# Kernel optimization log

Hardware: AMD Instinct MI355X
Metric: run time of the kernel (lower is better)

Reference implementation:

```python
import jax, jax.numpy as jnp
import numpy as np

G = 4      # num_groups
I = 128    # per-group input dim  (input_dim // num_groups)
H = 128    # per-group hidden dim (hidden_dim // num_groups)
B, T = 32, 1000


def setup_inputs() -> dict:
    key = jax.random.key(0)
    k0, k1, k2, k3, k4 = jax.random.split(key, 5)
    s = 1.0 / np.sqrt(H)  # PyTorch GRU init scale
    x = jax.random.normal(k0, (B, T, G * I), dtype=jnp.float32)
    w_ih = jax.random.uniform(k1, (G, 3 * H, I), jnp.float32, -s, s)
    w_hh = jax.random.uniform(k2, (G, 3 * H, H), jnp.float32, -s, s)
    b_ih = jax.random.uniform(k3, (G, 3 * H), jnp.float32, -s, s)
    b_hh = jax.random.uniform(k4, (G, 3 * H), jnp.float32, -s, s)
    return {"x": x, "w_ih": w_ih, "w_hh": w_hh, "b_ih": b_ih, "b_hh": b_hh}


def reference(x, w_ih, w_hh, b_ih, b_hh):
    # x: [B, T, G*I]. Chunking along dim 2 == reshape to [B, T, G, I].
    Bx, Tx, _ = x.shape
    xg = x.reshape(Bx, Tx, G, I)
    # Precompute input projections for all timesteps/groups (block-diagonal GEMM).
    gi = jnp.einsum('btgi,gki->btgk', xg, w_ih) + b_ih  # [B, T, G, 3H]

    def step(h, gi_t):
        # h: [B, G, H]; gi_t: [B, G, 3H]
        gh = jnp.einsum('bgh,gkh->bgk', h, w_hh) + b_hh  # [B, G, 3H]
        i_r, i_z, i_n = jnp.split(gi_t, 3, axis=-1)
        h_r, h_z, h_n = jnp.split(gh, 3, axis=-1)
        r = jax.nn.sigmoid(i_r + h_r)
        z = jax.nn.sigmoid(i_z + h_z)
        n = jnp.tanh(i_n + r * h_n)
        h_new = (1.0 - z) * n + z * h
        return h_new, h_new

    h0 = jnp.zeros((Bx, G, H), dtype=x.dtype)
    _, ys = jax.lax.scan(step, h0, jnp.swapaxes(gi, 0, 1))  # [T, B, G, H]
    # Concat of group outputs along dim 2 == reshape [B, T, G*H].
    return jnp.swapaxes(ys, 0, 1).reshape(Bx, Tx, G * H)
```

## Files before the change

### kernel.cpp

```cpp
#include <hip/hip_runtime.h>
#include <hip/hip_bf16.h>

#define NG 4
#define ID 128
#define HD 128
#define TH 384
#define NB 32
#define NT 1000
#define XW (NG*ID)
#define OW (NG*HD)

typedef _Float16 v8h __attribute__((ext_vector_type(8)));
typedef __attribute__((ext_vector_type(4))) float v4f;

__device__ __forceinline__ float sigm(float v) {
    return __fdividef(1.f, 1.f + __expf(-v));
}
__device__ __forceinline__ float tanh_(float v) {
    v = fminf(fmaxf(v, -15.f), 15.f);
    float e2 = __expf(2.f * v);
    return __fdividef(e2 - 1.f, e2 + 1.f);
}
__device__ __forceinline__ float sel4(v4f a, int s) {
    float x01 = (s & 1) ? a[1] : a[0];
    float x23 = (s & 1) ? a[3] : a[2];
    return (s & 2) ? x23 : x01;
}

__global__ __launch_bounds__(256) void gi_gemm4(
    const float* __restrict__ x,
    const float* __restrict__ w_ih,
    const float* __restrict__ b_ih,
    _Float16* __restrict__ gi_ws)
{
    const int tid = threadIdx.x;
    const int w   = tid >> 6, l = tid & 63;
    const int lr  = l & 15, lq = l >> 4;
    const int g   = blockIdx.z;
    const int b   = blockIdx.y >> 3;
    const int tt  = blockIdx.y & 7;
    const int gate = blockIdx.x;
    const int n0  = gate * 128 + (w >> 1) * 64;
    const int t0  = tt * 128 + (w & 1) * 64;

    v4f acc[4][4];
    #pragma unroll
    for (int mi = 0; mi < 4; ++mi)
        #pragma unroll
        for (int ni = 0; ni < 4; ++ni)
            acc[mi][ni] = (v4f){0.f, 0.f, 0.f, 0.f};

    #pragma unroll
    for (int kf = 0; kf < 4; ++kf) {
        v8h bf[4], af[4];
        #pragma unroll
        for (int ni = 0; ni < 4; ++ni) {
            const float* p = &w_ih[(size_t)(g * TH + n0 + ni * 16 + lr) * ID + kf * 32 + lq * 8];
            float4 f0 = *reinterpret_cast<const float4*>(p);
            float4 f1 = *reinterpret_cast<const float4*>(p + 4);
            v8h v;
            v[0]=(_Float16)f0.x; v[1]=(_Float16)f0.y; v[2]=(_Float16)f0.z; v[3]=(_Float16)f0.w;
            v[4]=(_Float16)f1.x; v[5]=(_Float16)f1.y; v[6]=(_Float16)f1.z; v[7]=(_Float16)f1.w;
            bf[ni] = v;
        }
        #pragma unroll
        for (int mi = 0; mi < 4; ++mi) {
            int trow = t0 + mi * 16 + lr;
            int tl = trow < NT ? trow : NT - 1;
            const float* p = &x[((size_t)b * NT + tl) * XW + g * ID + kf * 32 + lq * 8];
            float4 f0 = *reinterpret_cast<const float4*>(p);
            float4 f1 = *reinterpret_cast<const float4*>(p + 4);
            v8h v;
            v[0]=(_Float16)f0.x; v[1]=(_Float16)f0.y; v[2]=(_Float16)f0.z; v[3]=(_Float16)f0.w;
            v[4]=(_Float16)f1.x; v[5]=(_Float16)f1.y; v[6]=(_Float16)f1.z; v[7]=(_Float16)f1.w;
            af[mi] = v;
        }
        #pragma unroll
        for (int mi = 0; mi < 4; ++mi)
            #pragma unroll
            for (int ni = 0; ni < 4; ++ni)
                acc[mi][ni] = __builtin_amdgcn_mfma_f32_16x16x32_f16(
                    af[mi], bf[ni], acc[mi][ni], 0, 0, 0);
    }

    const size_t rbase = (size_t)(b * NG + g) * NT;
    #pragma unroll
    for (int ni = 0; ni < 4; ++ni) {
        const int col = n0 + ni * 16 + lr;
        const float bias = b_ih[g * TH + col];
        const int jj = col & 127;
        const int off = (gate == 0) ? jj * 2 : (gate == 1) ? jj * 2 + 1 : 256 + jj;
        #pragma unroll
        for (int mi = 0; mi < 4; ++mi) {
            #pragma unroll
            for (int r = 0; r < 4; ++r) {
                const int t = t0 + mi * 16 + lq * 4 + r;
                if (t < NT)
                    gi_ws[(rbase + t) * 384 + off] = (_Float16)(acc[mi][ni][r] + bias);
            }
        }
    }
}

__global__ __launch_bounds__(512) void gru_rec9(
    const _Float16* __restrict__ gi_ws,
    const float* __restrict__ w_hh,
    const float* __restrict__ b_hh,
    float* __restrict__ out)
{
    __shared__ __align__(16) _Float16 h_lds[2][128];

    const int tid = threadIdx.x;
    const int w = tid >> 6, l = tid & 63;
    const int lr = l & 15, lq = l >> 4;
    const int g = blockIdx.x & 3;
    const int b = blockIdx.x >> 2;

    v8h a[3][4];
    #pragma unroll
    for (int i = 0; i < 3; ++i) {
        const int mrow = i * 128 + 16 * w + lr;
        #pragma unroll
        for (int kf = 0; kf < 4; ++kf) {
            const float* p = &w_hh[(size_t)(g * TH + mrow) * HD + kf * 32 + lq * 8];
            float4 f0 = *reinterpret_cast<const float4*>(p);
            float4 f1 = *reinterpret_cast<const float4*>(p + 4);
            v8h v;
            v[0]=(_Float16)f0.x; v[1]=(_Float16)f0.y; v[2]=(_Float16)f0.z; v[3]=(_Float16)f0.w;
            v[4]=(_Float16)f1.x; v[5]=(_Float16)f1.y; v[6]=(_Float16)f1.z; v[7]=(_Float16)f1.w;
            a[i][kf] = v;
        }
    }

    const int sel = l & 3;
    const int j   = 16 * w + 4 * lq + sel;
    const bool active = ((l >> 2) & 3) == 0;
    const v4f bv0 = *reinterpret_cast<const v4f*>(&b_hh[g * TH +       16 * w + 4 * lq]);
    const v4f bv1 = *reinterpret_cast<const v4f*>(&b_hh[g * TH + 128 + 16 * w + 4 * lq]);
    const v4f bv2 = *reinterpret_cast<const v4f*>(&b_hh[g * TH + 256 + 16 * w + 4 * lq]);
    float hprev = 0.f;
    float* outp = out + (size_t)b * NT * OW + g * HD + j;

    if (tid < 128) { h_lds[0][tid] = (_Float16)0.f; h_lds[1][tid] = (_Float16)0.f; }

    const _Float16* gsrc = gi_ws + (size_t)(b * NG + g) * NT * 384;

    unsigned int rz0, rz1;
    _Float16 nv0, nv1;
    {
        const _Float16* g0 = gsrc;
        const _Float16* g1 = gsrc + 384;
        rz0 = *reinterpret_cast<const unsigned int*>(g0 + j * 2);
        nv0 = g0[256 + j];
        rz1 = *reinterpret_cast<const unsigned int*>(g1 + j * 2);
        nv1 = g1[256 + j];
    }
    __syncthreads();

#define STEP(P, TCUR, RZ, NV)                                                      \
    {                                                                              \
        const char* hb = reinterpret_cast<const char*>(&h_lds[P][0]) + lq * 16;    \
        v8h f0 = *reinterpret_cast<const v8h*>(hb);                                \
        v8h f1 = *reinterpret_cast<const v8h*>(hb + 64);                           \
        v8h f2 = *reinterpret_cast<const v8h*>(hb + 128);                          \
        v8h f3 = *reinterpret_cast<const v8h*>(hb + 192);                          \
        v4f ac0 = bv0, ac1 = bv1, ac2 = bv2;                                       \
        ac0 = __builtin_amdgcn_mfma_f32_16x16x32_f16(a[0][0], f0, ac0, 0, 0, 0);   \
        ac1 = __builtin_amdgcn_mfma_f32_16x16x32_f16(a[1][0], f0, ac1, 0, 0, 0);   \
        ac2 = __builtin_amdgcn_mfma_f32_16x16x32_f16(a[2][0], f0, ac2, 0, 0, 0);   \
        ac0 = __builtin_amdgcn_mfma_f32_16x16x32_f16(a[0][1], f1, ac0, 0, 0, 0);   \
        ac1 = __builtin_amdgcn_mfma_f32_16x16x32_f16(a[1][1], f1, ac1, 0, 0, 0);   \
        ac2 = __builtin_amdgcn_mfma_f32_16x16x32_f16(a[2][1], f1, ac2, 0, 0, 0);   \
        ac0 = __builtin_amdgcn_mfma_f32_16x16x32_f16(a[0][2], f2, ac0, 0, 0, 0);   \
        ac1 = __builtin_amdgcn_mfma_f32_16x16x32_f16(a[1][2], f2, ac1, 0, 0, 0);   \
        ac2 = __builtin_amdgcn_mfma_f32_16x16x32_f16(a[2][2], f2, ac2, 0, 0, 0);   \
        ac0 = __builtin_amdgcn_mfma_f32_16x16x32_f16(a[0][3], f3, ac0, 0, 0, 0);   \
        ac1 = __builtin_amdgcn_mfma_f32_16x16x32_f16(a[1][3], f3, ac1, 0, 0, 0);   \
        ac2 = __builtin_amdgcn_mfma_f32_16x16x32_f16(a[2][3], f3, ac2, 0, 0, 0);   \
        float ghr = sel4(ac0, sel);                                                \
        float ghz = sel4(ac1, sel);                                                \
        float ghn = sel4(ac2, sel);                                                \
        float iR = (float)__builtin_bit_cast(_Float16, (unsigned short)(RZ & 0xffff)); \
        float iZ = (float)__builtin_bit_cast(_Float16, (unsigned short)(RZ >> 16));    \
        float iN = (float)NV;                                                      \
        float rr = sigm(iR + ghr);                                                 \
        float zz = sigm(iZ + ghz);                                                 \
        float nn = tanh_(fmaf(rr, ghn, iN));                                       \
        float hn = fmaf(zz, hprev - nn, nn);                                       \
        hprev = hn;                                                                \
        if (active) {                                                              \
            h_lds[(P) ^ 1][j] = (_Float16)hn;                                      \
            outp[(size_t)(TCUR) * OW] = hn;                                        \
        }                                                                          \
        {                         \
            int tl = (TCUR) + 2 < NT ? (TCUR) + 2 : NT - 1;                        \
            const _Float16* gt = gsrc + (size_t)tl * 384;                          \
            RZ = *reinterpret_cast<const unsigned int*>(gt + j * 2);               \
            NV = gt[256 + j];                                                      \
        }                                                                          \
        asm volatile("s_waitcnt lgkmcnt(0)" ::: "memory");                         \
        __builtin_amdgcn_s_barrier();                                              \
        __builtin_amdgcn_sched_barrier(0);                                         \
    }

    for (int t = 0; t < NT; t += 2) {
        STEP(0, t,     rz0, nv0)
        STEP(1, t + 1, rz1, nv1)
    }
#undef STEP
}

extern "C" void kernel_launch(void* const* d_in, const int* in_sizes, int n_in,
                              void* d_out, int out_size, void* d_ws, size_t ws_size,
                              hipStream_t stream) {
    const float* x    = (const float*)d_in[0];
    const float* w_ih = (const float*)d_in[1];
    const float* w_hh = (const float*)d_in[2];
    const float* b_ih = (const float*)d_in[3];
    const float* b_hh = (const float*)d_in[4];
    float* out = (float*)d_out;
    _Float16* gi_ws = (_Float16*)d_ws;

    dim3 g1(3, NB * 8, NG);
    gi_gemm4<<<g1, 256, 0, stream>>>(x, w_ih, b_ih, gi_ws);
    gru_rec9<<<NB * NG, 512, 0, stream>>>(gi_ws, w_hh, b_hh, out);
}
```

Baseline: 555.8 us.

## Split MFMA accumulation chains, defer output stores, peel prefetch loop in GRU recurrence

```diff
diff --git a/kernel.cpp b/kernel.cpp
--- a/kernel.cpp
+++ b/kernel.cpp
@@ -102,7 +102,7 @@
     }
 }
 
-__global__ __launch_bounds__(512) void gru_rec9(
+__global__ __launch_bounds__(512) void gru_recA(
     const _Float16* __restrict__ gi_ws,
     const float* __restrict__ w_hh,
     const float* __restrict__ b_hh,
@@ -138,76 +138,81 @@
     const v4f bv0 = *reinterpret_cast<const v4f*>(&b_hh[g * TH +       16 * w + 4 * lq]);
     const v4f bv1 = *reinterpret_cast<const v4f*>(&b_hh[g * TH + 128 + 16 * w + 4 * lq]);
     const v4f bv2 = *reinterpret_cast<const v4f*>(&b_hh[g * TH + 256 + 16 * w + 4 * lq]);
-    float hprev = 0.f;
-    float* outp = out + (size_t)b * NT * OW + g * HD + j;
+    const v4f zv  = (v4f){0.f, 0.f, 0.f, 0.f};
+    float hprev = 0.f, pend = 0.f;
+    float* ostore = out + (size_t)b * NT * OW + g * HD + j - OW;
 
     if (tid < 128) { h_lds[0][tid] = (_Float16)0.f; h_lds[1][tid] = (_Float16)0.f; }
 
-    const _Float16* gsrc = gi_ws + (size_t)(b * NG + g) * NT * 384;
+    const char* gsrc = reinterpret_cast<const char*>(
+        gi_ws + (size_t)(b * NG + g) * NT * 384);
+    const int off_rz = j * 4;
+    const int off_nv = 512 + j * 2;
 
     unsigned int rz0, rz1;
     _Float16 nv0, nv1;
-    {
-        const _Float16* g0 = gsrc;
-        const _Float16* g1 = gsrc + 384;
-        rz0 = *reinterpret_cast<const unsigned int*>(g0 + j * 2);
-        nv0 = g0[256 + j];
-        rz1 = *reinterpret_cast<const unsigned int*>(g1 + j * 2);
-        nv1 = g1[256 + j];
-    }
+    rz0 = *reinterpret_cast<const unsigned int*>(gsrc + off_rz);
+    nv0 = *reinterpret_cast<const _Float16*>(gsrc + off_nv);
+    rz1 = *reinterpret_cast<const unsigned int*>(gsrc + 768 + off_rz);
+    nv1 = *reinterpret_cast<const _Float16*>(gsrc + 768 + off_nv);
+    const char* pEb = gsrc + 2 * 768;
+    const char* pOb = gsrc + 3 * 768;
     __syncthreads();
 
-#define STEP(P, TCUR, RZ, NV)                                                      \
+#define MM(AC, I, K, F) AC = __builtin_amdgcn_mfma_f32_16x16x32_f16(a[I][K], F, AC, 0, 0, 0)
+
+#define STEP(P, RZ, NV, PPTR, DO_PF, DO_ST)                                        \
     {                                                                              \
         const char* hb = reinterpret_cast<const char*>(&h_lds[P][0]) + lq * 16;    \
         v8h f0 = *reinterpret_cast<const v8h*>(hb);                                \
+        v8h f2 = *reinterpret_cast<const v8h*>(hb + 128);                          \
         v8h f1 = *reinterpret_cast<const v8h*>(hb + 64);                           \
-        v8h f2 = *reinterpret_cast<const v8h*>(hb + 128);                          \
         v8h f3 = *reinterpret_cast<const v8h*>(hb + 192);                          \
-        v4f ac0 = bv0, ac1 = bv1, ac2 = bv2;                                       \
-        ac0 = __builtin_amdgcn_mfma_f32_16x16x32_f16(a[0][0], f0, ac0, 0, 0, 0);   \
-        ac1 = __builtin_amdgcn_mfma_f32_16x16x32_f16(a[1][0], f0, ac1, 0, 0, 0);   \
-        ac2 = __builtin_amdgcn_mfma_f32_16x16x32_f16(a[2][0], f0, ac2, 0, 0, 0);   \
-        ac0 = __builtin_amdgcn_mfma_f32_16x16x32_f16(a[0][1], f1, ac0, 0, 0, 0);   \
-        ac1 = __builtin_amdgcn_mfma_f32_16x16x32_f16(a[1][1], f1, ac1, 0, 0, 0);   \
-        ac2 = __builtin_amdgcn_mfma_f32_16x16x32_f16(a[2][1], f1, ac2, 0, 0, 0);   \
-        ac0 = __builtin_amdgcn_mfma_f32_16x16x32_f16(a[0][2], f2, ac0, 0, 0, 0);   \
-        ac1 = __builtin_amdgcn_mfma_f32_16x16x32_f16(a[1][2], f2, ac1, 0, 0, 0);   \
-        ac2 = __builtin_amdgcn_mfma_f32_16x16x32_f16(a[2][2], f2, ac2, 0, 0, 0);   \
-        ac0 = __builtin_amdgcn_mfma_f32_16x16x32_f16(a[0][3], f3, ac0, 0, 0, 0);   \
-        ac1 = __builtin_amdgcn_mfma_f32_16x16x32_f16(a[1][3], f3, ac1, 0, 0, 0);   \
-        ac2 = __builtin_amdgcn_mfma_f32_16x16x32_f16(a[2][3], f3, ac2, 0, 0, 0);   \
+                        \
+        float iR = (float)__builtin_bit_cast(_Float16, (unsigned short)(RZ & 0xffff)); \
+        float iZ = (float)__builtin_bit_cast(_Float16, (unsigned short)(RZ >> 16));    \
+        float iN = (float)NV;                                                      \
+        if (DO_ST && active) *ostore = pend;                                       \
+        ostore += OW;                                                              \
+        if (DO_PF) {                                                               \
+            RZ = *reinterpret_cast<const unsigned int*>(PPTR + off_rz);            \
+            NV = *reinterpret_cast<const _Float16*>(PPTR + off_nv);                \
+            PPTR += 1536;                                                          \
+        }                                                                          \
+        __builtin_amdgcn_sched_barrier(0);                                         \
+        v4f c0a = bv0, c1a = bv1, c2a = bv2;                                       \
+        v4f c0b = zv,  c1b = zv,  c2b = zv;                                        \
+        MM(c0a, 0, 0, f0); MM(c1a, 1, 0, f0); MM(c2a, 2, 0, f0);                   \
+        MM(c0b, 0, 2, f2); MM(c1b, 1, 2, f2); MM(c2b, 2, 2, f2);                   \
+        MM(c0a, 0, 1, f1); MM(c1a, 1, 1, f1); MM(c2a, 2, 1, f1);                   \
+        MM(c0b, 0, 3, f3); MM(c1b, 1, 3, f3); MM(c2b, 2, 3, f3);                   \
+        v4f ac0 = c0a + c0b, ac1 = c1a + c1b, ac2 = c2a + c2b;                     \
         float ghr = sel4(ac0, sel);                                                \
         float ghz = sel4(ac1, sel);                                                \
         float ghn = sel4(ac2, sel);                                                \
-        float iR = (float)__builtin_bit_cast(_Float16, (unsigned short)(RZ & 0xffff)); \
-        float iZ = (float)__builtin_bit_cast(_Float16, (unsigned short)(RZ >> 16));    \
-        float iN = (float)NV;                                                      \
         float rr = sigm(iR + ghr);                                                 \
         float zz = sigm(iZ + ghz);                                                 \
         float nn = tanh_(fmaf(rr, ghn, iN));                                       \
         float hn = fmaf(zz, hprev - nn, nn);                                       \
         hprev = hn;                                                                \
-        if (active) {                                                              \
-            h_lds[(P) ^ 1][j] = (_Float16)hn;                                      \
-            outp[(size_t)(TCUR) * OW] = hn;                                        \
-        }                                                                          \
-        {                         \
-            int tl = (TCUR) + 2 < NT ? (TCUR) + 2 : NT - 1;                        \
-            const _Float16* gt = gsrc + (size_t)tl * 384;                          \
-            RZ = *reinterpret_cast<const unsigned int*>(gt + j * 2);               \
-            NV = gt[256 + j];                                                      \
-        }                                                                          \
+        pend = hn;                                                                 \
+        if (active) h_lds[(P) ^ 1][j] = (_Float16)hn;                              \
         asm volatile("s_waitcnt lgkmcnt(0)" ::: "memory");                         \
         __builtin_amdgcn_s_barrier();                                              \
         __builtin_amdgcn_sched_barrier(0);                                         \
     }
 
-    for (int t = 0; t < NT; t += 2) {
-        STEP(0, t,     rz0, nv0)
-        STEP(1, t + 1, rz1, nv1)
-    }
+    STEP(0, rz0, nv0, pEb, 1, 0)
+    STEP(1, rz1, nv1, pOb, 1, 1)
+    for (int t = 2; t < NT - 2; t += 2) {
+        STEP(0, rz0, nv0, pEb, 1, 1)
+        STEP(1, rz1, nv1, pOb, 1, 1)
+    }
+    STEP(0, rz0, nv0, pEb, 0, 1)
+    STEP(1, rz1, nv1, pOb, 0, 1)
+    if (active) *ostore = pend;
 #undef STEP
+#undef MM
 }
 
 extern "C" void kernel_launch(void* const* d_in, const int* in_sizes, int n_in,
@@ -223,5 +228,5 @@
 
     dim3 g1(3, NB * 8, NG);
     gi_gemm4<<<g1, 256, 0, stream>>>(x, w_ih, b_ih, gi_ws);
-    gru_rec9<<<NB * NG, 512, 0, stream>>>(gi_ws, w_hh, b_hh, out);
-}
+    gru_recA<<<NB * NG, 512, 0, stream>>>(gi_ws, w_hh, b_hh, out);
+}
```

Result: slower. 669.8 us (+20.5%).

## Fuse input projection GEMM into recurrent GRU kernel, precomputing only fp16 x

Applied to the files above, without the earlier changes.

```diff
diff --git a/kernel.cpp b/kernel.cpp
--- a/kernel.cpp
+++ b/kernel.cpp
@@ -27,84 +27,26 @@
     return (s & 2) ? x23 : x01;
 }
 
-__global__ __launch_bounds__(256) void gi_gemm4(
-    const float* __restrict__ x,
-    const float* __restrict__ w_ih,
-    const float* __restrict__ b_ih,
-    _Float16* __restrict__ gi_ws)
+__global__ __launch_bounds__(128) void x_cvt(
+    const float* __restrict__ x, _Float16* __restrict__ x16)
 {
+    const int b = blockIdx.x, t = blockIdx.y;
     const int tid = threadIdx.x;
-    const int w   = tid >> 6, l = tid & 63;
-    const int lr  = l & 15, lq = l >> 4;
-    const int g   = blockIdx.z;
-    const int b   = blockIdx.y >> 3;
-    const int tt  = blockIdx.y & 7;
-    const int gate = blockIdx.x;
-    const int n0  = gate * 128 + (w >> 1) * 64;
-    const int t0  = tt * 128 + (w & 1) * 64;
-
-    v4f acc[4][4];
-    #pragma unroll
-    for (int mi = 0; mi < 4; ++mi)
-        #pragma unroll
-        for (int ni = 0; ni < 4; ++ni)
-            acc[mi][ni] = (v4f){0.f, 0.f, 0.f, 0.f};
-
-    #pragma unroll
-    for (int kf = 0; kf < 4; ++kf) {
-        v8h bf[4], af[4];
-        #pragma unroll
-        for (int ni = 0; ni < 4; ++ni) {
-            const float* p = &w_ih[(size_t)(g * TH + n0 + ni * 16 + lr) * ID + kf * 32 + lq * 8];
-            float4 f0 = *reinterpret_cast<const float4*>(p);
-            float4 f1 = *reinterpret_cast<const float4*>(p + 4);
-            v8h v;
-            v[0]=(_Float16)f0.x; v[1]=(_Float16)f0.y; v[2]=(_Float16)f0.z; v[3]=(_Float16)f0.w;
-            v[4]=(_Float16)f1.x; v[5]=(_Float16)f1.y; v[6]=(_Float16)f1.z; v[7]=(_Float16)f1.w;
-            bf[ni] = v;
-        }
-        #pragma unroll
-        for (int mi = 0; mi < 4; ++mi) {
-            int trow = t0 + mi * 16 + lr;
-            int tl = trow < NT ? trow : NT - 1;
-            const float* p = &x[((size_t)b * NT + tl) * XW + g * ID + kf * 32 + lq * 8];
-            float4 f0 = *reinterpret_cast<const float4*>(p);
-            float4 f1 = *reinterpret_cast<const float4*>(p + 4);
-            v8h v;
-            v[0]=(_Float16)f0.x; v[1]=(_Float16)f0.y; v[2]=(_Float16)f0.z; v[3]=(_Float16)f0.w;
-            v[4]=(_Float16)f1.x; v[5]=(_Float16)f1.y; v[6]=(_Float16)f1.z; v[7]=(_Float16)f1.w;
-            af[mi] = v;
-        }
-        #pragma unroll
-        for (int mi = 0; mi < 4; ++mi)
-            #pragma unroll
-            for (int ni = 0; ni < 4; ++ni)
-                acc[mi][ni] = __builtin_amdgcn_mfma_f32_16x16x32_f16(
-                    af[mi], bf[ni], acc[mi][ni], 0, 0, 0);
-    }
-
-    const size_t rbase = (size_t)(b * NG + g) * NT;
-    #pragma unroll
-    for (int ni = 0; ni < 4; ++ni) {
-        const int col = n0 + ni * 16 + lr;
-        const float bias = b_ih[g * TH + col];
-        const int jj = col & 127;
-        const int off = (gate == 0) ? jj * 2 : (gate == 1) ? jj * 2 + 1 : 256 + jj;
-        #pragma unroll
-        for (int mi = 0; mi < 4; ++mi) {
-            #pragma unroll
-            for (int r = 0; r < 4; ++r) {
-                const int t = t0 + mi * 16 + lq * 4 + r;
-                if (t < NT)
-                    gi_ws[(rbase + t) * 384 + off] = (_Float16)(acc[mi][ni][r] + bias);
-            }
-        }
-    }
+    const int g = tid >> 5, cc = (tid & 31) * 4;
+    float4 v = *reinterpret_cast<const float4*>(
+        &x[((size_t)b * NT + t) * XW + g * ID + cc]);
+    union { _Float16 h[4]; uint2 u; } pk;
+    pk.h[0] = (_Float16)v.x; pk.h[1] = (_Float16)v.y;
+    pk.h[2] = (_Float16)v.z; pk.h[3] = (_Float16)v.w;
+    *reinterpret_cast<uint2*>(
+        &x16[(((size_t)b * NG + g) * NT + t) * ID + cc]) = pk.u;
 }
 
-__global__ __launch_bounds__(512) void gru_rec9(
-    const _Float16* __restrict__ gi_ws,
+__global__ __launch_bounds__(512) void gru_recD(
+    const _Float16* __restrict__ x16,
+    const float* __restrict__ w_ih,
     const float* __restrict__ w_hh,
+    const float* __restrict__ b_ih,
     const float* __restrict__ b_hh,
     float* __restrict__ out)
 {
@@ -116,7 +58,7 @@
     const int g = blockIdx.x & 3;
     const int b = blockIdx.x >> 2;
 
-    v8h a[3][4];
+    v8h aH[3][4], aI[3][4];
     #pragma unroll
     for (int i = 0; i < 3; ++i) {
         const int mrow = i * 128 + 16 * w + lr;
@@ -128,61 +70,73 @@
             v8h v;
             v[0]=(_Float16)f0.x; v[1]=(_Float16)f0.y; v[2]=(_Float16)f0.z; v[3]=(_Float16)f0.w;
             v[4]=(_Float16)f1.x; v[5]=(_Float16)f1.y; v[6]=(_Float16)f1.z; v[7]=(_Float16)f1.w;
-            a[i][kf] = v;
+            aH[i][kf] = v;
+            const float* q = &w_ih[(size_t)(g * TH + mrow) * ID + kf * 32 + lq * 8];
+            float4 g0 = *reinterpret_cast<const float4*>(q);
+            float4 g1 = *reinterpret_cast<const float4*>(q + 4);
+            v8h u;
+            u[0]=(_Float16)g0.x; u[1]=(_Float16)g0.y; u[2]=(_Float16)g0.z; u[3]=(_Float16)g0.w;
+            u[4]=(_Float16)g1.x; u[5]=(_Float16)g1.y; u[6]=(_Float16)g1.z; u[7]=(_Float16)g1.w;
+            aI[i][kf] = u;
         }
     }
 
     const int sel = l & 3;
     const int j   = 16 * w + 4 * lq + sel;
     const bool active = ((l >> 2) & 3) == 0;
-    const v4f bv0 = *reinterpret_cast<const v4f*>(&b_hh[g * TH +       16 * w + 4 * lq]);
-    const v4f bv1 = *reinterpret_cast<const v4f*>(&b_hh[g * TH + 128 + 16 * w + 4 * lq]);
-    const v4f bv2 = *reinterpret_cast<const v4f*>(&b_hh[g * TH + 256 + 16 * w + 4 * lq]);
+    const v4f bh0 = *reinterpret_cast<const v4f*>(&b_hh[g * TH +       16 * w + 4 * lq]);
+    const v4f bh1 = *reinterpret_cast<const v4f*>(&b_hh[g * TH + 128 + 16 * w + 4 * lq]);
+    const v4f bh2 = *reinterpret_cast<const v4f*>(&b_hh[g * TH + 256 + 16 * w + 4 * lq]);
+    const v4f bi0 = *reinterpret_cast<const v4f*>(&b_ih[g * TH +       16 * w + 4 * lq]);
+    const v4f bi1 = *reinterpret_cast<const v4f*>(&b_ih[g * TH + 128 + 16 * w + 4 * lq]);
+    const v4f bi2 = *reinterpret_cast<const v4f*>(&b_ih[g * TH + 256 + 16 * w + 4 * lq]);
     float hprev = 0.f;
     float* outp = out + (size_t)b * NT * OW + g * HD + j;
 
     if (tid < 128) { h_lds[0][tid] = (_Float16)0.f; h_lds[1][tid] = (_Float16)0.f; }
 
-    const _Float16* gsrc = gi_ws + (size_t)(b * NG + g) * NT * 384;
-
-    unsigned int rz0, rz1;
-    _Float16 nv0, nv1;
-    {
-        const _Float16* g0 = gsrc;
-        const _Float16* g1 = gsrc + 384;
-        rz0 = *reinterpret_cast<const unsigned int*>(g0 + j * 2);
-        nv0 = g0[256 + j];
-        rz1 = *reinterpret_cast<const unsigned int*>(g1 + j * 2);
-        nv1 = g1[256 + j];
-    }
+    const char* xbase = reinterpret_cast<const char*>(
+        x16 + ((size_t)(b * NG + g)) * NT * ID);
+    const int fo = lq * 16;
+    v8h xe0, xe1, xe2, xe3, xo0, xo1, xo2, xo3;
+    xe0 = *reinterpret_cast<const v8h*>(xbase +   0 + fo);
+    xe1 = *reinterpret_cast<const v8h*>(xbase +  64 + fo);
+    xe2 = *reinterpret_cast<const v8h*>(xbase + 128 + fo);
+    xe3 = *reinterpret_cast<const v8h*>(xbase + 192 + fo);
+    xo0 = *reinterpret_cast<const v8h*>(xbase + 256 + fo);
+    xo1 = *reinterpret_cast<const v8h*>(xbase + 320 + fo);
+    xo2 = *reinterpret_cast<const v8h*>(xbase + 384 + fo);
+    xo3 = *reinterpret_cast<const v8h*>(xbase + 448 + fo);
+    const char* pxE = xbase + 2 * 256;
+    const char* pxO = xbase + 3 * 256;
     __syncthreads();
 
-#define STEP(P, TCUR, RZ, NV)                                                      \
+#define MM(AC, AF, K, F) AC = __builtin_amdgcn_mfma_f32_16x16x32_f16(AF[K], F, AC, 0, 0, 0)
+
+#define STEP(P, X0, X1, X2, X3, PX, DO_PF)                                         \
     {                                                                              \
-        const char* hb = reinterpret_cast<const char*>(&h_lds[P][0]) + lq * 16;    \
+        const char* hb = reinterpret_cast<const char*>(&h_lds[P][0]) + fo;         \
         v8h f0 = *reinterpret_cast<const v8h*>(hb);                                \
         v8h f1 = *reinterpret_cast<const v8h*>(hb + 64);                           \
         v8h f2 = *reinterpret_cast<const v8h*>(hb + 128);                          \
         v8h f3 = *reinterpret_cast<const v8h*>(hb + 192);                          \
-        v4f ac0 = bv0, ac1 = bv1, ac2 = bv2;                                       \
-        ac0 = __builtin_amdgcn_mfma_f32_16x16x32_f16(a[0][0], f0, ac0, 0, 0, 0);   \
-        ac1 = __builtin_amdgcn_mfma_f32_16x16x32_f16(a[1][0], f0, ac1, 0, 0, 0);   \
-        ac2 = __builtin_amdgcn_mfma_f32_16x16x32_f16(a[2][0], f0, ac2, 0, 0, 0);   \
-        ac0 = __builtin_amdgcn_mfma_f32_16x16x32_f16(a[0][1], f1, ac0, 0, 0, 0);   \
-        ac1 = __builtin_amdgcn_mfma_f32_16x16x32_f16(a[1][1], f1, ac1, 0, 0, 0);   \
-        ac2 = __builtin_amdgcn_mfma_f32_16x16x32_f16(a[2][1], f1, ac2, 0, 0, 0);   \
-        ac0 = __builtin_amdgcn_mfma_f32_16x16x32_f16(a[0][2], f2, ac0, 0, 0, 0);   \
-        ac1 = __builtin_amdgcn_mfma_f32_16x16x32_f16(a[1][2], f2, ac1, 0, 0, 0);   \
-        ac2 = __builtin_amdgcn_mfma_f32_16x16x32_f16(a[2][2], f2, ac2, 0, 0, 0);   \
-        ac0 = __builtin_amdgcn_mfma_f32_16x16x32_f16(a[0][3], f3, ac0, 0, 0, 0);   \
-        ac1 = __builtin_amdgcn_mfma_f32_16x16x32_f16(a[1][3], f3, ac1, 0, 0, 0);   \
-        ac2 = __builtin_amdgcn_mfma_f32_16x16x32_f16(a[2][3], f3, ac2, 0, 0, 0);   \
-        float ghr = sel4(ac0, sel);                                                \
-        float ghz = sel4(ac1, sel);                                                \
-        float ghn = sel4(ac2, sel);                                                \
-        float iR = (float)__builtin_bit_cast(_Float16, (unsigned short)(RZ & 0xffff)); \
-        float iZ = (float)__builtin_bit_cast(_Float16, (unsigned short)(RZ >> 16));    \
-        float iN = (float)NV;                                                      \
+               \
+        v4f i0 = bi0, i1 = bi1, i2 = bi2;                                          \
+        MM(i0, aI[0], 0, X0); MM(i1, aI[1], 0, X0); MM(i2, aI[2], 0, X0);          \
+        MM(i0, aI[0], 1, X1); MM(i1, aI[1], 1, X1); MM(i2, aI[2], 1, X1);          \
+        MM(i0, aI[0], 2, X2); MM(i1, aI[1], 2, X2); MM(i2, aI[2], 2, X2);          \
+        MM(i0, aI[0], 3, X3); MM(i1, aI[1], 3, X3); MM(i2, aI[2], 3, X3);          \
+        v4f c0 = bh0, c1 = bh1, c2 = bh2;                                          \
+        MM(c0, aH[0], 0, f0); MM(c1, aH[1], 0, f0); MM(c2, aH[2], 0, f0);          \
+        MM(c0, aH[0], 1, f1); MM(c1, aH[1], 1, f1); MM(c2, aH[2], 1, f1);          \
+        MM(c0, aH[0], 2, f2); MM(c1, aH[1], 2, f2); MM(c2, aH[2], 2, f2);          \
+        MM(c0, aH[0], 3, f3); MM(c1, aH[1], 3, f3); MM(c2, aH[2], 3, f3);          \
+        float iR = sel4(i0, sel);                                                  \
+        float iZ = sel4(i1, sel);                                                  \
+        float iN = sel4(i2, sel);                                                  \
+        float ghr = sel4(c0, sel);                                                 \
+        float ghz = sel4(c1, sel);                                                 \
+        float ghn = sel4(c2, sel);                                                 \
         float rr = sigm(iR + ghr);                                                 \
         float zz = sigm(iZ + ghz);                                                 \
         float nn = tanh_(fmaf(rr, ghn, iN));                                       \
@@ -190,24 +144,29 @@
         hprev = hn;                                                                \
         if (active) {                                                              \
             h_lds[(P) ^ 1][j] = (_Float16)hn;                                      \
-            outp[(size_t)(TCUR) * OW] = hn;                                        \
+            *outp = hn;                                                            \
         }                                                                          \
-        {                         \
-            int tl = (TCUR) + 2 < NT ? (TCUR) + 2 : NT - 1;                        \
-            const _Float16* gt = gsrc + (size_t)tl * 384;                          \
-            RZ = *reinterpret_cast<const unsigned int*>(gt + j * 2);               \
-            NV = gt[256 + j];                                                      \
+        outp += OW;                                                                \
+        if (DO_PF) {                                                               \
+            X0 = *reinterpret_cast<const v8h*>(PX +   0 + fo);                     \
+            X1 = *reinterpret_cast<const v8h*>(PX +  64 + fo);                     \
+            X2 = *reinterpret_cast<const v8h*>(PX + 128 + fo);                     \
+            X3 = *reinterpret_cast<const v8h*>(PX + 192 + fo);                     \
+            PX += 512;                                                             \
         }                                                                          \
         asm volatile("s_waitcnt lgkmcnt(0)" ::: "memory");                         \
         __builtin_amdgcn_s_barrier();                                              \
         __builtin_amdgcn_sched_barrier(0);                                         \
     }
 
-    for (int t = 0; t < NT; t += 2) {
-        STEP(0, t,     rz0, nv0)
-        STEP(1, t + 1, rz1, nv1)
+    for (int t = 0; t < NT - 2; t += 2) {
+        STEP(0, xe0, xe1, xe2, xe3, pxE, 1)
+        STEP(1, xo0, xo1, xo2, xo3, pxO, 1)
     }
+    STEP(0, xe0, xe1, xe2, xe3, pxE, 0)
+    STEP(1, xo0, xo1, xo2, xo3, pxO, 0)
 #undef STEP
+#undef MM
 }
 
 extern "C" void kernel_launch(void* const* d_in, const int* in_sizes, int n_in,
@@ -219,9 +178,9 @@
     const float* b_ih = (const float*)d_in[3];
     const float* b_hh = (const float*)d_in[4];
     float* out = (float*)d_out;
-    _Float16* gi_ws = (_Float16*)d_ws;
+    _Float16* x16 = (_Float16*)d_ws;
 
-    dim3 g1(3, NB * 8, NG);
-    gi_gemm4<<<g1, 256, 0, stream>>>(x, w_ih, b_ih, gi_ws);
-    gru_rec9<<<NB * NG, 512, 0, stream>>>(gi_ws, w_hh, b_hh, out);
+    dim3 gc(NB, NT);
+    x_cvt<<<gc, 128, 0, stream>>>(x, x16);
+    gru_recD<<<NB * NG, 512, 0, stream>>>(x16, w_ih, w_hh, b_ih, b_hh, out);
 }
```

After: 633.4 us. +14.0%, slower.
